# Performance work log

Hardware: AMD Instinct MI355X
Metric: run time of the kernel (lower is better)

## Reference

```python
import jax, jax.numpy as jnp
import numpy as np
import math

B, L, E, H = 4, 4096, 2048, 16
HD = E // H  # 128

def setup_inputs() -> dict:
    key = jax.random.key(0)
    k1, k2, k3, k4, k5 = jax.random.split(key, 5)
    s = 1.0 / math.sqrt(E)
    return {
        "x": jax.random.normal(k1, (B, L, E), dtype=jnp.float32),
        "Wq": jax.random.normal(k2, (E, E), dtype=jnp.float32) * s,
        "bq": jax.random.normal(k3, (E,), dtype=jnp.float32) * s,
        "Wkv": jax.random.normal(k4, (2 * HD, E), dtype=jnp.float32) * s,
        "bkv": jax.random.normal(k5, (2 * HD,), dtype=jnp.float32) * s,
    }

def reference(x, Wq, bq, Wkv, bkv):
    b, l, e = x.shape
    hd = Wkv.shape[0] // 2
    h = e // hd
    q = (x @ Wq.T + bq).reshape(b, l, h, hd)          # [B,L,H,hd]
    kv = (x @ Wkv.T + bkv).reshape(b, l, 2, hd)
    k, v = kv[:, :, 0], kv[:, :, 1]                   # [B,L,hd] each
    # Faithful to source: q @ k.unsqueeze(2).transpose(-2,-1) -> [B,L,H,1]
    attn = jnp.einsum('blhd,bld->blh', q, k)[..., None] / math.sqrt(hd)
    attn = jax.nn.softmax(attn, axis=-1)              # size-1 axis -> all ones
    # attn @ v.unsqueeze(2): [B,L,H,1] @ [B,L,1,hd] -> [B,L,H,hd]
    out = (attn * v[:, :, None, :]).reshape(b, l, -1)  # [B,L,E]
    return out
```

## Files before the change

kernel.cpp:

```cpp
#include <hip/hip_runtime.h>


typedef __attribute__((ext_vector_type(8))) short bf16x8;
typedef __attribute__((ext_vector_type(4))) float f32x4;

#define M_TOTAL 16384
#define K_DIM   2048
#define BM      16
#define BK      64
#define NT      (K_DIM / BK)
#define TILE_BYTES 20480
#define NBUF    4

__device__ __forceinline__ unsigned short f2bf(float f) {
    unsigned int u = __float_as_uint(f);
    u += 0x7FFFu + ((u >> 16) & 1u);
    return (unsigned short)(u >> 16);
}

#define GLOAD_LDS16(gp, lp) __builtin_amdgcn_global_load_lds( \
    (const __attribute__((address_space(1))) void*)(gp),      \
    (__attribute__((address_space(3))) void*)(lp), 16, 0, 0)

#define WAITV(N) asm volatile("s_waitcnt vmcnt(" #N ")" ::: "memory")
#define BAR() do { asm volatile("" ::: "memory"); __builtin_amdgcn_s_barrier(); \
                   asm volatile("" ::: "memory"); } while (0)

__global__ void prep_wv(const float* __restrict__ Wkv, unsigned short* __restrict__ Wvp) {
    const int tid = blockIdx.x * 256 + threadIdx.x;
    const int l  = tid & 63;
    const int cb = (tid >> 6) & 15;
    const int t  = tid >> 10;
    const int c  = cb & 7, ks = cb >> 3;
    const int col   = c * 16 + (l & 15);
    const int kbase = t * 64 + ks * 32 + (l >> 4) * 8;
    const float* src = Wkv + (size_t)(128 + col) * K_DIM + kbase;
    const float4 f0 = *reinterpret_cast<const float4*>(src);
    const float4 f1 = *reinterpret_cast<const float4*>(src + 4);
    ushort4 o0 = { f2bf(f0.x), f2bf(f0.y), f2bf(f0.z), f2bf(f0.w) };
    ushort4 o1 = { f2bf(f1.x), f2bf(f1.y), f2bf(f1.z), f2bf(f1.w) };
    ushort4* dst = reinterpret_cast<ushort4*>(Wvp + (size_t)tid * 8);
    dst[0] = o0; dst[1] = o1;
}

__global__ __launch_bounds__(256, 2) void mqa_v_gemm(
    const float* __restrict__ x,
    const unsigned short* __restrict__ Wvp,
    const float* __restrict__ bkv,
    float* __restrict__ out)
{
    __shared__ __align__(16) char smem[NBUF * TILE_BYTES];

    const int tid  = threadIdx.x;
    const int l    = tid & 63;
    const int w    = tid >> 6;
    const int frow = l & 15;
    const int fg   = l >> 4;
    const size_t row0 = (size_t)blockIdx.x * BM;

    const int srow   = w * 4 + (l >> 4);
    const int scol16 = frow ^ (srow & 7);
    const float* gA = x + (row0 + srow) * K_DIM + scol16 * 4;

    #define STAGE(t, buf) do {                                            \
        char* tb_ = smem + (buf) * TILE_BYTES;                            \
        GLOAD_LDS16(gA + (t) * BK, tb_ + w * 1024);                       \
        const unsigned short* gb_ = Wvp + (size_t)(t) * 8192 + w * 512 + l * 8; \
        GLOAD_LDS16(gb_,        tb_ + 4096 + (w     ) * 1024);            \
        GLOAD_LDS16(gb_ + 2048, tb_ + 4096 + (w +  4) * 1024);            \
        GLOAD_LDS16(gb_ + 4096, tb_ + 4096 + (w +  8) * 1024);            \
        GLOAD_LDS16(gb_ + 6144, tb_ + 4096 + (w + 12) * 1024);            \
    } while (0)

    f32x4 acc0 = {0.f, 0.f, 0.f, 0.f};
    f32x4 acc1 = {0.f, 0.f, 0.f, 0.f};

    #define COMPUTE(t) do {                                               \
        const char* tb_ = smem + ((t) & (NBUF - 1)) * TILE_BYTES;         \
        const char* Ab_ = tb_;                                            \
        const char* Bb_ = tb_ + 4096;                                     \
        _Pragma("unroll")                                                 \
        for (int ks = 0; ks < 2; ++ks) {                                  \
            float4 af0 = *reinterpret_cast<const float4*>(                \
                Ab_ + frow * 256 + (((ks * 8 + fg * 2 + 0) ^ (frow & 7)) << 4)); \
            float4 af1 = *reinterpret_cast<const float4*>(                \
                Ab_ + frow * 256 + (((ks * 8 + fg * 2 + 1) ^ (frow & 7)) << 4)); \
            union { unsigned int u[4]; bf16x8 v; } a_;                    \
            asm("v_cvt_pk_bf16_f32 %0, %1, %2" : "=v"(a_.u[0]) : "v"(af0.x), "v"(af0.y)); \
            asm("v_cvt_pk_bf16_f32 %0, %1, %2" : "=v"(a_.u[1]) : "v"(af0.z), "v"(af0.w)); \
            asm("v_cvt_pk_bf16_f32 %0, %1, %2" : "=v"(a_.u[2]) : "v"(af1.x), "v"(af1.y)); \
            asm("v_cvt_pk_bf16_f32 %0, %1, %2" : "=v"(a_.u[3]) : "v"(af1.z), "v"(af1.w)); \
            bf16x8 b0 = *reinterpret_cast<const bf16x8*>(                 \
                Bb_ + (ks * 8 + 2 * w    ) * 1024 + l * 16);              \
            bf16x8 b1 = *reinterpret_cast<const bf16x8*>(                 \
                Bb_ + (ks * 8 + 2 * w + 1) * 1024 + l * 16);              \
            acc0 = __builtin_amdgcn_mfma_f32_16x16x32_bf16(a_.v, b0, acc0, 0, 0, 0); \
            acc1 = __builtin_amdgcn_mfma_f32_16x16x32_bf16(a_.v, b1, acc1, 0, 0, 0); \
        }                                                                 \
    } while (0)

    STAGE(0, 0);
    STAGE(1, 1);

    for (int t = 0; t < NT - 2; ++t) {
        STAGE(t + 2, (t + 2) & (NBUF - 1));
        WAITV(10);
        BAR();
        COMPUTE(t);
    }
    WAITV(5);
    BAR();
    COMPUTE(NT - 2);
    WAITV(0);
    BAR();
    COMPUTE(NT - 1);

    float* vl = reinterpret_cast<float*>(smem);
    const int c0 = w * 32 + frow;
    const int c1 = c0 + 16;
    const float bias0 = bkv[128 + c0];
    const float bias1 = bkv[128 + c1];
    #pragma unroll
    for (int j = 0; j < 4; ++j) {
        const int r = fg * 4 + j;
        vl[r * 132 + c0] = acc0[j] + bias0;
        vl[r * 132 + c1] = acc1[j] + bias1;
    }
    __syncthreads();

    float4* op = reinterpret_cast<float4*>(out + row0 * K_DIM);
    #pragma unroll
    for (int i = tid; i < BM * (K_DIM / 4); i += 256) {
        const int r  = i >> 9;
        const int c4 = i & 511;
        op[i] = *reinterpret_cast<const float4*>(vl + r * 132 + (c4 & 31) * 4);
    }
}

extern "C" void kernel_launch(void* const* d_in, const int* in_sizes, int n_in,
                              void* d_out, int out_size, void* d_ws, size_t ws_size,
                              hipStream_t stream)
{
    const float* x   = (const float*)d_in[0];
    const float* Wkv = (const float*)d_in[3];
    const float* bkv = (const float*)d_in[4];
    float* out       = (float*)d_out;
    unsigned short* Wvp = (unsigned short*)d_ws;

    prep_wv<<<128, 256, 0, stream>>>(Wkv, Wvp);
    mqa_v_gemm<<<M_TOTAL / BM, 256, 0, stream>>>(x, Wvp, bkv, out);
}
```

Measured before the change: 266.3 us.

## Replace LDS-staged pipelined GEMM with direct global-to-register loads

The 4-stage LDS ring buffer fed by global_load_lds, along with its waitcnt/barrier schedule, is removed. Each wave now loads its x fragments and packed bf16 Wv fragments straight from global memory into registers, and the loop is unrolled by 4. This cuts LDS use, so occupancy can rise and the barrier stalls go away. In exchange, each of the four waves re-reads the same x rows from global or L2 (fourfold redundant x traffic), and latency is hidden only by unrolling and occupancy rather than an explicit prefetch.

```diff
diff --git a/kernel.cpp b/kernel.cpp
--- a/kernel.cpp
+++ b/kernel.cpp
@@ -7,24 +7,13 @@
 #define M_TOTAL 16384
 #define K_DIM   2048
 #define BM      16
-#define BK      64
-#define NT      (K_DIM / BK)
-#define TILE_BYTES 20480
-#define NBUF    4
+#define NT      32
 
 __device__ __forceinline__ unsigned short f2bf(float f) {
     unsigned int u = __float_as_uint(f);
     u += 0x7FFFu + ((u >> 16) & 1u);
     return (unsigned short)(u >> 16);
 }
-
-#define GLOAD_LDS16(gp, lp) __builtin_amdgcn_global_load_lds( \
-    (const __attribute__((address_space(1))) void*)(gp),      \
-    (__attribute__((address_space(3))) void*)(lp), 16, 0, 0)
-
-#define WAITV(N) asm volatile("s_waitcnt vmcnt(" #N ")" ::: "memory")
-#define BAR() do { asm volatile("" ::: "memory"); __builtin_amdgcn_s_barrier(); \
-                   asm volatile("" ::: "memory"); } while (0)
 
 __global__ void prep_wv(const float* __restrict__ Wkv, unsigned short* __restrict__ Wvp) {
     const int tid = blockIdx.x * 256 + threadIdx.x;
@@ -43,13 +32,22 @@
     dst[0] = o0; dst[1] = o1;
 }
 
-__global__ __launch_bounds__(256, 2) void mqa_v_gemm(
+__device__ __forceinline__ bf16x8 cvt_frag(float4 lo, float4 hi) {
+    union { unsigned int u[4]; bf16x8 v; } r;
+    asm("v_cvt_pk_bf16_f32 %0, %1, %2" : "=v"(r.u[0]) : "v"(lo.x), "v"(lo.y));
+    asm("v_cvt_pk_bf16_f32 %0, %1, %2" : "=v"(r.u[1]) : "v"(lo.z), "v"(lo.w));
+    asm("v_cvt_pk_bf16_f32 %0, %1, %2" : "=v"(r.u[2]) : "v"(hi.x), "v"(hi.y));
+    asm("v_cvt_pk_bf16_f32 %0, %1, %2" : "=v"(r.u[3]) : "v"(hi.z), "v"(hi.w));
+    return r.v;
+}
+
+__global__ __launch_bounds__(256) void mqa_v_gemm(
     const float* __restrict__ x,
     const unsigned short* __restrict__ Wvp,
     const float* __restrict__ bkv,
     float* __restrict__ out)
 {
-    __shared__ __align__(16) char smem[NBUF * TILE_BYTES];
+    __shared__ __align__(16) float vl[BM][132];
 
     const int tid  = threadIdx.x;
     const int l    = tid & 63;
@@ -58,64 +56,33 @@
     const int fg   = l >> 4;
     const size_t row0 = (size_t)blockIdx.x * BM;
 
-    const int srow   = w * 4 + (l >> 4);
-    const int scol16 = frow ^ (srow & 7);
-    const float* gA = x + (row0 + srow) * K_DIM + scol16 * 4;
-
-    #define STAGE(t, buf) do {                                            \
-        char* tb_ = smem + (buf) * TILE_BYTES;                            \
-        GLOAD_LDS16(gA + (t) * BK, tb_ + w * 1024);                       \
-        const unsigned short* gb_ = Wvp + (size_t)(t) * 8192 + w * 512 + l * 8; \
-        GLOAD_LDS16(gb_,        tb_ + 4096 + (w     ) * 1024);            \
-        GLOAD_LDS16(gb_ + 2048, tb_ + 4096 + (w +  4) * 1024);            \
-        GLOAD_LDS16(gb_ + 4096, tb_ + 4096 + (w +  8) * 1024);            \
-        GLOAD_LDS16(gb_ + 6144, tb_ + 4096 + (w + 12) * 1024);            \
-    } while (0)
+    const float* gA = x + (row0 + frow) * (size_t)K_DIM + fg * 8;
+    const unsigned short* gB = Wvp + (size_t)l * 8;
 
     f32x4 acc0 = {0.f, 0.f, 0.f, 0.f};
     f32x4 acc1 = {0.f, 0.f, 0.f, 0.f};
 
-    #define COMPUTE(t) do {                                               \
-        const char* tb_ = smem + ((t) & (NBUF - 1)) * TILE_BYTES;         \
-        const char* Ab_ = tb_;                                            \
-        const char* Bb_ = tb_ + 4096;                                     \
-        _Pragma("unroll")                                                 \
-        for (int ks = 0; ks < 2; ++ks) {                                  \
-            float4 af0 = *reinterpret_cast<const float4*>(                \
-                Ab_ + frow * 256 + (((ks * 8 + fg * 2 + 0) ^ (frow & 7)) << 4)); \
-            float4 af1 = *reinterpret_cast<const float4*>(                \
-                Ab_ + frow * 256 + (((ks * 8 + fg * 2 + 1) ^ (frow & 7)) << 4)); \
-            union { unsigned int u[4]; bf16x8 v; } a_;                    \
-            asm("v_cvt_pk_bf16_f32 %0, %1, %2" : "=v"(a_.u[0]) : "v"(af0.x), "v"(af0.y)); \
-            asm("v_cvt_pk_bf16_f32 %0, %1, %2" : "=v"(a_.u[1]) : "v"(af0.z), "v"(af0.w)); \
-            asm("v_cvt_pk_bf16_f32 %0, %1, %2" : "=v"(a_.u[2]) : "v"(af1.x), "v"(af1.y)); \
-            asm("v_cvt_pk_bf16_f32 %0, %1, %2" : "=v"(a_.u[3]) : "v"(af1.z), "v"(af1.w)); \
-            bf16x8 b0 = *reinterpret_cast<const bf16x8*>(                 \
-                Bb_ + (ks * 8 + 2 * w    ) * 1024 + l * 16);              \
-            bf16x8 b1 = *reinterpret_cast<const bf16x8*>(                 \
-                Bb_ + (ks * 8 + 2 * w + 1) * 1024 + l * 16);              \
-            acc0 = __builtin_amdgcn_mfma_f32_16x16x32_bf16(a_.v, b0, acc0, 0, 0, 0); \
-            acc1 = __builtin_amdgcn_mfma_f32_16x16x32_bf16(a_.v, b1, acc1, 0, 0, 0); \
-        }                                                                 \
-    } while (0)
+    #pragma unroll 4
+    for (int t = 0; t < NT; ++t) {
+        const float* at = gA + t * 64;
+        const float4 a0lo = *reinterpret_cast<const float4*>(at);
+        const float4 a0hi = *reinterpret_cast<const float4*>(at + 4);
+        const float4 a1lo = *reinterpret_cast<const float4*>(at + 32);
+        const float4 a1hi = *reinterpret_cast<const float4*>(at + 36);
+        const bf16x8 b00 = *reinterpret_cast<const bf16x8*>(gB + ((t * 16 +     2 * w    ) << 9));
+        const bf16x8 b01 = *reinterpret_cast<const bf16x8*>(gB + ((t * 16 +     2 * w + 1) << 9));
+        const bf16x8 b10 = *reinterpret_cast<const bf16x8*>(gB + ((t * 16 + 8 + 2 * w    ) << 9));
+        const bf16x8 b11 = *reinterpret_cast<const bf16x8*>(gB + ((t * 16 + 8 + 2 * w + 1) << 9));
 
-    STAGE(0, 0);
-    STAGE(1, 1);
+        const bf16x8 a0 = cvt_frag(a0lo, a0hi);
+        const bf16x8 a1 = cvt_frag(a1lo, a1hi);
 
-    for (int t = 0; t < NT - 2; ++t) {
-        STAGE(t + 2, (t + 2) & (NBUF - 1));
-        WAITV(10);
-        BAR();
-        COMPUTE(t);
+        acc0 = __builtin_amdgcn_mfma_f32_16x16x32_bf16(a0, b00, acc0, 0, 0, 0);
+        acc1 = __builtin_amdgcn_mfma_f32_16x16x32_bf16(a0, b01, acc1, 0, 0, 0);
+        acc0 = __builtin_amdgcn_mfma_f32_16x16x32_bf16(a1, b10, acc0, 0, 0, 0);
+        acc1 = __builtin_amdgcn_mfma_f32_16x16x32_bf16(a1, b11, acc1, 0, 0, 0);
     }
-    WAITV(5);
-    BAR();
-    COMPUTE(NT - 2);
-    WAITV(0);
-    BAR();
-    COMPUTE(NT - 1);
 
-    float* vl = reinterpret_cast<float*>(smem);
     const int c0 = w * 32 + frow;
     const int c1 = c0 + 16;
     const float bias0 = bkv[128 + c0];
@@ -123,8 +90,8 @@
     #pragma unroll
     for (int j = 0; j < 4; ++j) {
         const int r = fg * 4 + j;
-        vl[r * 132 + c0] = acc0[j] + bias0;
-        vl[r * 132 + c1] = acc1[j] + bias1;
+        vl[r][c0] = acc0[j] + bias0;
+        vl[r][c1] = acc1[j] + bias1;
     }
     __syncthreads();
 
@@ -132,8 +99,8 @@
     #pragma unroll
     for (int i = tid; i < BM * (K_DIM / 4); i += 256) {
         const int r  = i >> 9;
-        const int c4 = i & 511;
-        op[i] = *reinterpret_cast<const float4*>(vl + r * 132 + (c4 & 31) * 4);
+        const int c4 = i & 31;
+        op[i] = *reinterpret_cast<const float4*>(&vl[r][c4 << 2]);
     }
 }
 
```

New measurement: 295.0 us. 10.8% more time.
